# Performance work log

Hardware: AMD Instinct MI355X
Metric: run time of the kernel (lower is better)

## Reference

```python
import jax, jax.numpy as jnp
import numpy as np

K_V = 0.5
G_OFF = 0.001
G_ON = 0.005
N_IN = 4096
N_OUT = 4096
BATCH = 8192


def setup_inputs() -> dict:
    key = jax.random.key(0)
    k1, k2, k3 = jax.random.split(key, 3)
    x = jax.random.normal(k1, (BATCH, N_IN), dtype=jnp.float32)
    # RandomNormal(stddev=1/sqrt(neurons_in)) initializer
    w = jax.random.normal(k2, (N_IN, N_OUT), dtype=jnp.float32) / np.sqrt(N_IN)
    # bias initialized to 0 in the module; use small noise so it is non-degenerate
    b = jax.random.normal(k3, (N_OUT,), dtype=jnp.float32) * 0.01
    return {"x": x, "w": w, "b": b}


def reference(x, w, b):
    # combine_weights: fold bias as an extra input row, x gets a ones column
    weights = jnp.concatenate([w, b[None, :]], axis=0)            # (n_in+1, n_out)
    ones = jnp.ones((x.shape[0], 1), dtype=x.dtype)
    voltages = K_V * jnp.concatenate([x, ones], axis=1)           # (B, n_in+1)

    # weights_to_conductances, 'lowest' mapping rule (differential pair)
    max_weight = jnp.max(jnp.abs(weights))
    k_cond = (G_ON - G_OFF) / max_weight
    g_eff = k_cond * weights
    g_pos = G_OFF + jnp.maximum(g_eff, 0.0)                       # even columns
    g_neg = G_OFF - jnp.minimum(g_eff, 0.0)                       # odd columns
    # interleave pos/neg -> (n_in+1, 2*n_out)
    conductances = jnp.stack([g_pos, g_neg], axis=-1).reshape(weights.shape[0], -1)

    # crossbar currents: scaled GEMM
    currents = voltages @ conductances                            # (B, 2*n_out)

    # differential current subtraction + rescale back to weight domain
    total_currents = currents[:, 0::2] - currents[:, 1::2]        # (B, n_out)
    y_disturbed = total_currents / (K_V * k_cond)
    return y_disturbed
```

## Files before the change

kernel.cpp:

```cpp
#include <hip/hip_runtime.h>
#include <cstdint>

typedef unsigned short u16;
typedef __attribute__((ext_vector_type(8))) __bf16 bf16x8;
typedef __attribute__((ext_vector_type(4))) float f32x4;

#define M_DIM 8192
#define N_DIM 4096
#define K_DIM 4096

__device__ __forceinline__ u16 f2bf(float f) {
    union { float f; uint32_t u; } v; v.f = f;
    uint32_t u = v.u;
    u += 0x7FFFu + ((u >> 16) & 1u);
    return (u16)(u >> 16);
}

__global__ __launch_bounds__(256) void cvt_x_kernel(const float* __restrict__ x,
                                                    u16* __restrict__ xb) {
    size_t i = ((size_t)blockIdx.x * 256 + threadIdx.x) * 8;
    const float4* p = (const float4*)(x + i);
    float4 v0 = p[0], v1 = p[1];
    uint32_t o0 = (uint32_t)f2bf(v0.x) | ((uint32_t)f2bf(v0.y) << 16);
    uint32_t o1 = (uint32_t)f2bf(v0.z) | ((uint32_t)f2bf(v0.w) << 16);
    uint32_t o2 = (uint32_t)f2bf(v1.x) | ((uint32_t)f2bf(v1.y) << 16);
    uint32_t o3 = (uint32_t)f2bf(v1.z) | ((uint32_t)f2bf(v1.w) << 16);
    uint4 o; o.x = o0; o.y = o1; o.z = o2; o.w = o3;
    *(uint4*)(xb + i) = o;
}

__global__ __launch_bounds__(256) void cvt_wt_kernel(const float* __restrict__ w,
                                                     u16* __restrict__ wt) {
    __shared__ u16 lds[64 * 66];
    const int t = threadIdx.x;
    const int k0 = blockIdx.x * 64;
    const int n0 = blockIdx.y * 64;
#pragma unroll
    for (int i = 0; i < 16; ++i) {
        int idx = i * 256 + t;
        int r = idx >> 6, c = idx & 63;
        lds[r * 66 + c] = f2bf(w[(size_t)(k0 + r) * N_DIM + n0 + c]);
    }
    __syncthreads();
#pragma unroll
    for (int i = 0; i < 8; ++i) {
        int idx = i * 256 + t;
        int rn = idx >> 5;
        int ck = (idx & 31) * 2;
        uint32_t lo = lds[ck * 66 + rn];
        uint32_t hi = lds[(ck + 1) * 66 + rn];
        *(uint32_t*)&wt[(size_t)(n0 + rn) * K_DIM + k0 + ck] = lo | (hi << 16);
    }
}

typedef const uint32_t __attribute__((address_space(1)))* gp_t;
typedef uint32_t __attribute__((address_space(3)))* lp_t;

__global__ __launch_bounds__(256) void gemm_kernel(const u16* __restrict__ A,
                                                   const u16* __restrict__ Bt,
                                                   const float* __restrict__ bias,
                                                   float* __restrict__ C) {
    __shared__ u16 As[128 * 32];
    __shared__ u16 Bs[128 * 32];

    const int t    = threadIdx.x;
    const int lane = t & 63;
    const int l16  = lane & 15;
    const int quad = lane >> 4;
    const int wave = t >> 6;
    const int wm   = (wave >> 1) * 64;
    const int wn   = (wave & 1) * 64;
    const int bm   = blockIdx.y * 128;
    const int bn   = blockIdx.x * 128;

    f32x4 acc[4][4] = {};

    const int c0 = t, c1 = 256 + t;
    const int rA0 = c0 >> 2, kc0 = (c0 & 3) * 8;
    const int rA1 = c1 >> 2, kc1 = (c1 & 3) * 8;
    const u16* a0 = A  + (size_t)(bm + rA0) * K_DIM + kc0;
    const u16* a1 = A  + (size_t)(bm + rA1) * K_DIM + kc1;
    const u16* b0 = Bt + (size_t)(bn + rA0) * K_DIM + kc0;
    const u16* b1 = Bt + (size_t)(bn + rA1) * K_DIM + kc1;

    for (int k0 = 0; k0 < K_DIM; k0 += 32) {
        __syncthreads();
        __builtin_amdgcn_global_load_lds((gp_t)(a0 + k0), (lp_t)&As[c0 * 8], 16, 0, 0);
        __builtin_amdgcn_global_load_lds((gp_t)(a1 + k0), (lp_t)&As[c1 * 8], 16, 0, 0);
        __builtin_amdgcn_global_load_lds((gp_t)(b0 + k0), (lp_t)&Bs[c0 * 8], 16, 0, 0);
        __builtin_amdgcn_global_load_lds((gp_t)(b1 + k0), (lp_t)&Bs[c1 * 8], 16, 0, 0);
        __syncthreads();

        bf16x8 af[4], bf[4];
#pragma unroll
        for (int i = 0; i < 4; ++i) {
            af[i] = *(const bf16x8*)&As[(wm + i * 16 + l16) * 32 + quad * 8];
            bf[i] = *(const bf16x8*)&Bs[(wn + i * 16 + l16) * 32 + quad * 8];
        }
#pragma unroll
        for (int i = 0; i < 4; ++i)
#pragma unroll
            for (int j = 0; j < 4; ++j)
                acc[i][j] = __builtin_amdgcn_mfma_f32_16x16x32_bf16(af[i], bf[j], acc[i][j], 0, 0, 0);
    }

#pragma unroll
    for (int j = 0; j < 4; ++j) {
        const int col = bn + wn + j * 16 + l16;
        const float bv = bias[col];
#pragma unroll
        for (int i = 0; i < 4; ++i) {
            const int row = bm + wm + i * 16 + quad * 4;
#pragma unroll
            for (int r = 0; r < 4; ++r)
                C[(size_t)(row + r) * N_DIM + col] = acc[i][j][r] + bv;
        }
    }
}

extern "C" void kernel_launch(void* const* d_in, const int* in_sizes, int n_in,
                              void* d_out, int out_size, void* d_ws, size_t ws_size,
                              hipStream_t stream) {
    const float* x = (const float*)d_in[0];
    const float* w = (const float*)d_in[1];
    const float* b = (const float*)d_in[2];
    float* out = (float*)d_out;

    u16* xb = (u16*)d_ws;
    u16* wt = xb + (size_t)M_DIM * K_DIM;

    cvt_x_kernel<<<(M_DIM * (size_t)K_DIM) / (256 * 8), 256, 0, stream>>>(x, xb);
    cvt_wt_kernel<<<dim3(K_DIM / 64, N_DIM / 64), 256, 0, stream>>>(w, wt);
    gemm_kernel<<<dim3(N_DIM / 128, M_DIM / 128), 256, 0, stream>>>(xb, wt, b, out);
}
```

Before: 572.8 us.

## Swizzle GEMM LDS layout, merge conversion kernels, vectorize weight transpose

```diff
diff --git a/kernel.cpp b/kernel.cpp
--- a/kernel.cpp
+++ b/kernel.cpp
@@ -9,6 +9,9 @@
 #define N_DIM 4096
 #define K_DIM 4096
 
+#define CVT_X_BLOCKS 16384
+#define CVT_W_BLOCKS 4096
+
 __device__ __forceinline__ u16 f2bf(float f) {
     union { float f; uint32_t u; } v; v.f = f;
     uint32_t u = v.u;
@@ -16,40 +19,48 @@
     return (u16)(u >> 16);
 }
 
-__global__ __launch_bounds__(256) void cvt_x_kernel(const float* __restrict__ x,
-                                                    u16* __restrict__ xb) {
-    size_t i = ((size_t)blockIdx.x * 256 + threadIdx.x) * 8;
-    const float4* p = (const float4*)(x + i);
-    float4 v0 = p[0], v1 = p[1];
-    uint32_t o0 = (uint32_t)f2bf(v0.x) | ((uint32_t)f2bf(v0.y) << 16);
-    uint32_t o1 = (uint32_t)f2bf(v0.z) | ((uint32_t)f2bf(v0.w) << 16);
-    uint32_t o2 = (uint32_t)f2bf(v1.x) | ((uint32_t)f2bf(v1.y) << 16);
-    uint32_t o3 = (uint32_t)f2bf(v1.z) | ((uint32_t)f2bf(v1.w) << 16);
-    uint4 o; o.x = o0; o.y = o1; o.z = o2; o.w = o3;
-    *(uint4*)(xb + i) = o;
-}
-
-__global__ __launch_bounds__(256) void cvt_wt_kernel(const float* __restrict__ w,
-                                                     u16* __restrict__ wt) {
-    __shared__ u16 lds[64 * 66];
+__global__ __launch_bounds__(256) void cvt_kernel(const float* __restrict__ x,
+                                                  const float* __restrict__ w,
+                                                  u16* __restrict__ xb,
+                                                  u16* __restrict__ wt) {
     const int t = threadIdx.x;
-    const int k0 = blockIdx.x * 64;
-    const int n0 = blockIdx.y * 64;
+    if (blockIdx.x < CVT_X_BLOCKS) {
+        size_t i = ((size_t)blockIdx.x * 256 + t) * 8;
+        const float4* p = (const float4*)(x + i);
+        float4 v0 = p[0], v1 = p[1];
+        uint32_t o0 = (uint32_t)f2bf(v0.x) | ((uint32_t)f2bf(v0.y) << 16);
+        uint32_t o1 = (uint32_t)f2bf(v0.z) | ((uint32_t)f2bf(v0.w) << 16);
+        uint32_t o2 = (uint32_t)f2bf(v1.x) | ((uint32_t)f2bf(v1.y) << 16);
+        uint32_t o3 = (uint32_t)f2bf(v1.z) | ((uint32_t)f2bf(v1.w) << 16);
+        uint4 o; o.x = o0; o.y = o1; o.z = o2; o.w = o3;
+        *(uint4*)(xb + i) = o;
+    } else {
+        __shared__ u16 lds[64 * 68];
+        const int bid = blockIdx.x - CVT_X_BLOCKS;
+        const int k0 = (bid & 63) * 64;
+        const int n0 = (bid >> 6) * 64;
 #pragma unroll
-    for (int i = 0; i < 16; ++i) {
-        int idx = i * 256 + t;
-        int r = idx >> 6, c = idx & 63;
-        lds[r * 66 + c] = f2bf(w[(size_t)(k0 + r) * N_DIM + n0 + c]);
-    }
-    __syncthreads();
+        for (int i = 0; i < 4; ++i) {
+            int idx = i * 256 + t;
+            int r = idx >> 4;
+            int c4 = (idx & 15) * 4;
+            float4 v = *(const float4*)&w[(size_t)(k0 + r) * N_DIM + n0 + c4];
+            uint2 o;
+            o.x = (uint32_t)f2bf(v.x) | ((uint32_t)f2bf(v.y) << 16);
+            o.y = (uint32_t)f2bf(v.z) | ((uint32_t)f2bf(v.w) << 16);
+            *(uint2*)&lds[r * 68 + c4] = o;
+        }
+        __syncthreads();
 #pragma unroll
-    for (int i = 0; i < 8; ++i) {
-        int idx = i * 256 + t;
-        int rn = idx >> 5;
-        int ck = (idx & 31) * 2;
-        uint32_t lo = lds[ck * 66 + rn];
-        uint32_t hi = lds[(ck + 1) * 66 + rn];
-        *(uint32_t*)&wt[(size_t)(n0 + rn) * K_DIM + k0 + ck] = lo | (hi << 16);
+        for (int i = 0; i < 4; ++i) {
+            int idx = i * 256 + t;
+            int rn  = idx >> 4;
+            int ck  = (idx & 15) * 4;
+            uint2 o;
+            o.x = (uint32_t)lds[(ck + 0) * 68 + rn] | ((uint32_t)lds[(ck + 1) * 68 + rn] << 16);
+            o.y = (uint32_t)lds[(ck + 2) * 68 + rn] | ((uint32_t)lds[(ck + 3) * 68 + rn] << 16);
+            *(uint2*)&wt[(size_t)(n0 + rn) * K_DIM + k0 + ck] = o;
+        }
     }
 }
 
@@ -76,12 +87,15 @@
     f32x4 acc[4][4] = {};
 
     const int c0 = t, c1 = 256 + t;
-    const int rA0 = c0 >> 2, kc0 = (c0 & 3) * 8;
-    const int rA1 = c1 >> 2, kc1 = (c1 & 3) * 8;
-    const u16* a0 = A  + (size_t)(bm + rA0) * K_DIM + kc0;
-    const u16* a1 = A  + (size_t)(bm + rA1) * K_DIM + kc1;
-    const u16* b0 = Bt + (size_t)(bn + rA0) * K_DIM + kc0;
-    const u16* b1 = Bt + (size_t)(bn + rA1) * K_DIM + kc1;
+    const int rA0 = c0 >> 2, rA1 = c1 >> 2;
+    const int sw  = ((rA0 >> 1) & 3);
+    const int kc  = ((c0 & 3) ^ sw) * 8;
+    const u16* a0 = A  + (size_t)(bm + rA0) * K_DIM + kc;
+    const u16* a1 = A  + (size_t)(bm + rA1) * K_DIM + kc;
+    const u16* b0 = Bt + (size_t)(bn + rA0) * K_DIM + kc;
+    const u16* b1 = Bt + (size_t)(bn + rA1) * K_DIM + kc;
+
+    const int sw8 = (quad ^ ((l16 >> 1) & 3)) * 8;
 
     for (int k0 = 0; k0 < K_DIM; k0 += 32) {
         __syncthreads();
@@ -94,8 +108,8 @@
         bf16x8 af[4], bf[4];
 #pragma unroll
         for (int i = 0; i < 4; ++i) {
-            af[i] = *(const bf16x8*)&As[(wm + i * 16 + l16) * 32 + quad * 8];
-            bf[i] = *(const bf16x8*)&Bs[(wn + i * 16 + l16) * 32 + quad * 8];
+            af[i] = *(const bf16x8*)&As[(wm + i * 16 + l16) * 32 + sw8];
+            bf[i] = *(const bf16x8*)&Bs[(wn + i * 16 + l16) * 32 + sw8];
         }
 #pragma unroll
         for (int i = 0; i < 4; ++i)
@@ -129,7 +143,6 @@
     u16* xb = (u16*)d_ws;
     u16* wt = xb + (size_t)M_DIM * K_DIM;
 
-    cvt_x_kernel<<<(M_DIM * (size_t)K_DIM) / (256 * 8), 256, 0, stream>>>(x, xb);
-    cvt_wt_kernel<<<dim3(K_DIM / 64, N_DIM / 64), 256, 0, stream>>>(w, wt);
+    cvt_kernel<<<CVT_X_BLOCKS + CVT_W_BLOCKS, 256, 0, stream>>>(x, w, xb, wt);
     gemm_kernel<<<dim3(N_DIM / 128, M_DIM / 128), 256, 0, stream>>>(xb, wt, b, out);
 }
```

New measurement: 566.4 us. About the same (-1.1%).
